# Optimization experiments

Measured on AMD Instinct MI355X. Metric: run time of the kernel, lower is better.

## Reference

```python
import jax, jax.numpy as jnp
import numpy as np

NC, NS, NX, NZ = 128, 2048, 256, 512
B, K = 4, 1
NNZ = NX * NZ * NC  # 16_777_216 nonzeros (~Nc contributions per pixel)


def setup_inputs() -> dict:
    key = jax.random.key(0)
    k1, k2, k3, k4 = jax.random.split(key, 4)
    x = jax.random.normal(k1, (B, K, NC, NS), dtype=jnp.float32)
    csr_vals = jax.random.normal(k2, (NNZ,), dtype=jnp.float32)
    csr_rows = jnp.sort(jax.random.randint(k3, (NNZ,), 0, NX * NZ, dtype=jnp.int64))
    csr_cols = jax.random.randint(k4, (NNZ,), 0, NS * NC, dtype=jnp.int64)
    return {"x": x, "csr_vals": csr_vals, "csr_rows": csr_rows, "csr_cols": csr_cols}


def reference(x, csr_vals, csr_rows, csr_cols):
    # (B,K,Nc,Ns) -> (B,K,Ns,Nc) -> (B*K, Ns*Nc) -> transpose -> (Ns*Nc, B*K)
    rhs = jnp.transpose(x, (0, 1, 3, 2)).reshape(B * K, NS * NC).T
    # SpMM in COO form: out[r, :] += vals * rhs[cols, :]
    gathered = csr_vals[:, None] * rhs[csr_cols]          # (nnz, B*K)
    img_vec = jax.ops.segment_sum(gathered, csr_rows, num_segments=NX * NZ)  # (Nx*Nz, B*K)
    # transpose -> (B*K, Nx*Nz) -> (B,K,Nx,Nz) -> (B,K,Nz,Nx)
    return jnp.transpose(img_vec.T.reshape(B, K, NX, NZ), (0, 1, 3, 2))
```

## Files before the change

kernel.cpp:

```cpp
#include <hip/hip_runtime.h>
#include <hip/hip_fp16.h>

#define NC 128
#define NS 2048
#define NX 256
#define NZ 512
#define NROWS (NX * NZ)
#define NCOLS (NS * NC)
#define RUN 8
#define WAVE_NNZ (RUN * 64)
#define NSLOTS 64


struct alignas(8) Half4 { __half2 lo, hi; };

typedef int   vint4   __attribute__((ext_vector_type(4)));
typedef float vfloat4 __attribute__((ext_vector_type(4)));

__device__ __forceinline__ int4 nt_load_i4(const int* p) {
    vint4 t = __builtin_nontemporal_load((const vint4*)p);
    return make_int4(t.x, t.y, t.z, t.w);
}
__device__ __forceinline__ float4 nt_load_f4(const float* p) {
    vfloat4 t = __builtin_nontemporal_load((const vfloat4*)p);
    return make_float4(t.x, t.y, t.z, t.w);
}

__global__ void pack_rhs_kernel(const float* __restrict__ x,
                                Half4* __restrict__ rhs) {
    int j = blockIdx.x * blockDim.x + threadIdx.x;
    if (j >= NCOLS) return;
    int c = j >> 11;
    int s = j & (NS - 1);
    int base = c * NS + s;
    Half4 h;
    h.lo = __float22half2_rn(make_float2(x[base],               x[base + 1 * NC * NS]));
    h.hi = __float22half2_rn(make_float2(x[base + 2 * NC * NS], x[base + 3 * NC * NS]));
    rhs[s * NC + c] = h;
}

__device__ __forceinline__ void global_flush(float* __restrict__ out, int r, float4 a) {
    int ix = r >> 9;
    int iz = r & (NZ - 1);
    int o = iz * NX + ix;
    atomicAdd(&out[0 * NROWS + o], a.x);
    atomicAdd(&out[1 * NROWS + o], a.y);
    atomicAdd(&out[2 * NROWS + o], a.z);
    atomicAdd(&out[3 * NROWS + o], a.w);
}

__global__ void __launch_bounds__(256, 8) spmm_seg_kernel(
        const float* __restrict__ vals,
        const int* __restrict__ cols,
        const int* __restrict__ rows,
        const Half4* __restrict__ rhs,
        float* __restrict__ out,
        int nnz) {
    __shared__ float sl[4][NSLOTS][4];

    int wv   = threadIdx.x >> 6;
    int lane = threadIdx.x & 63;
    int wid  = (blockIdx.x << 2) + wv;
    int base = wid * WAVE_NNZ + lane * RUN;

    ((float4*)sl)[threadIdx.x] = make_float4(0.f, 0.f, 0.f, 0.f);
    __syncthreads();

    float4 v[2];
    int4   c4[2], r4[2];
    if (base + RUN <= nnz) {
        #pragma unroll
        for (int q = 0; q < 2; ++q) c4[q] = nt_load_i4(cols + base + 4 * q);
        #pragma unroll
        for (int q = 0; q < 2; ++q) v[q]  = nt_load_f4(vals + base + 4 * q);
        #pragma unroll
        for (int q = 0; q < 2; ++q) r4[q] = nt_load_i4(rows + base + 4 * q);
    } else {
        #pragma unroll
        for (int q = 0; q < 2; ++q) {
            #pragma unroll
            for (int k = 0; k < 4; ++k) {
                int e = base + 4 * q + k;
                int ec = e < nnz ? e : (nnz - 1);
                (&v[q].x)[k]  = e < nnz ? vals[ec] : 0.f;
                (&c4[q].x)[k] = cols[ec];
                (&r4[q].x)[k] = rows[ec];
            }
        }
    }

    Half4 g[RUN];
    #pragma unroll
    for (int q = 0; q < 2; ++q) {
        g[4 * q + 0] = rhs[c4[q].x];
        g[4 * q + 1] = rhs[c4[q].y];
        g[4 * q + 2] = rhs[c4[q].z];
        g[4 * q + 3] = rhs[c4[q].w];
    }
    __builtin_amdgcn_sched_barrier(0);

    int rfirst = __shfl(r4[0].x, 0);
    int rlast  = __shfl(r4[1].w, 63);

    int cur = r4[0].x;
    float4 acc = make_float4(0.f, 0.f, 0.f, 0.f);
    #pragma unroll
    for (int j = 0; j < RUN; ++j) {
        int   rj = (&r4[j >> 2].x)[j & 3];
        float vj = (&v[j >> 2].x)[j & 3];
        float2 lo = __half22float2(g[j].lo);
        float2 hi = __half22float2(g[j].hi);
        if (rj != cur) {
            int s = cur - rfirst;
            if (s < NSLOTS) {
                atomicAdd(&sl[wv][s][0], acc.x);
                atomicAdd(&sl[wv][s][1], acc.y);
                atomicAdd(&sl[wv][s][2], acc.z);
                atomicAdd(&sl[wv][s][3], acc.w);
            } else {
                global_flush(out, cur, acc);
            }
            acc = make_float4(0.f, 0.f, 0.f, 0.f);
            cur = rj;
        }
        acc.x += vj * lo.x;
        acc.y += vj * lo.y;
        acc.z += vj * hi.x;
        acc.w += vj * hi.y;
    }
    {
        int s = cur - rfirst;
        if (s < NSLOTS) {
            atomicAdd(&sl[wv][s][0], acc.x);
            atomicAdd(&sl[wv][s][1], acc.y);
            atomicAdd(&sl[wv][s][2], acc.z);
            atomicAdd(&sl[wv][s][3], acc.w);
        } else {
            global_flush(out, cur, acc);
        }
    }

    __syncthreads();

    int span = rlast - rfirst;
    if (lane <= span && lane < NSLOTS) {
        float ax = sl[wv][lane][0];
        float ay = sl[wv][lane][1];
        float az = sl[wv][lane][2];
        float aw = sl[wv][lane][3];
        int rr = rfirst + lane;
        int ix = rr >> 9;
        int iz = rr & (NZ - 1);
        int o = iz * NX + ix;
        if (lane == 0 || rr == rlast) {
            atomicAdd(&out[0 * NROWS + o], ax);
            atomicAdd(&out[1 * NROWS + o], ay);
            atomicAdd(&out[2 * NROWS + o], az);
            atomicAdd(&out[3 * NROWS + o], aw);
        } else {
            out[0 * NROWS + o] = ax;
            out[1 * NROWS + o] = ay;
            out[2 * NROWS + o] = az;
            out[3 * NROWS + o] = aw;
        }
    }
}

__global__ void __launch_bounds__(256) spmm_direct_kernel(
        const float* __restrict__ x,
        const float* __restrict__ vals,
        const int* __restrict__ rows,
        const int* __restrict__ cols,
        int nnz,
        float* __restrict__ out) {
    int r = (blockIdx.x << 2) + (threadIdx.x >> 6);
    int lane = threadIdx.x & 63;
    int start, end;
    {
        int lo = 0, hi = nnz;
        while (lo < hi) { int mid = (lo + hi) >> 1; if (rows[mid] < r) lo = mid + 1; else hi = mid; }
        start = lo;
        hi = nnz;
        int key = r + 1;
        while (lo < hi) { int mid = (lo + hi) >> 1; if (rows[mid] < key) lo = mid + 1; else hi = mid; }
        end = lo;
    }
    float4 acc = {0.f, 0.f, 0.f, 0.f};
    for (int i = start + lane; i < end; i += 64) {
        float v = vals[i];
        int col = cols[i];
        int cc = col & (NC - 1);
        int ss = col >> 7;
        int b = cc * NS + ss;
        acc.x += v * x[b];
        acc.y += v * x[b + 1 * NC * NS];
        acc.z += v * x[b + 2 * NC * NS];
        acc.w += v * x[b + 3 * NC * NS];
    }
    #pragma unroll
    for (int off = 32; off >= 1; off >>= 1) {
        acc.x += __shfl_xor(acc.x, off, 64);
        acc.y += __shfl_xor(acc.y, off, 64);
        acc.z += __shfl_xor(acc.z, off, 64);
        acc.w += __shfl_xor(acc.w, off, 64);
    }
    if (lane < 4) {
        float o = (lane == 0) ? acc.x : (lane == 1) ? acc.y : (lane == 2) ? acc.z : acc.w;
        int ix = r >> 9;
        int iz = r & (NZ - 1);
        out[lane * NROWS + iz * NX + ix] = o;
    }
}

extern "C" void kernel_launch(void* const* d_in, const int* in_sizes, int n_in,
                              void* d_out, int out_size, void* d_ws, size_t ws_size,
                              hipStream_t stream) {
    const float* x        = (const float*)d_in[0];
    const float* csr_vals = (const float*)d_in[1];
    const int*   csr_rows = (const int*)d_in[2];
    const int*   csr_cols = (const int*)d_in[3];
    float* out = (float*)d_out;
    int nnz = in_sizes[1];

    size_t need = (size_t)NCOLS * sizeof(Half4);
    if (ws_size >= need) {
        Half4* rhs = (Half4*)d_ws;
        hipMemsetAsync(out, 0, (size_t)out_size * sizeof(float), stream);
        pack_rhs_kernel<<<(NCOLS + 255) / 256, 256, 0, stream>>>(x, rhs);
        int nblocks = (nnz + 4 * WAVE_NNZ - 1) / (4 * WAVE_NNZ);
        spmm_seg_kernel<<<nblocks, 256, 0, stream>>>(csr_vals, csr_cols, csr_rows,
                                                     rhs, out, nnz);
    } else {
        spmm_direct_kernel<<<NROWS / 4, 256, 0, stream>>>(x, csr_vals, csr_rows, csr_cols, nnz, out);
    }
}
```

Before: 287.6 us.

## Software-pipeline four nnz tiles per wave with double-buffered loads and gathers

Each wave now processes four consecutive 512-nonzero tiles instead of one. The index and value stream loads and the rhs gathers for the next tile are issued before accumulating the current one, using two register buffers. The block-wide barrier is dropped because each wave uses only its own shared-memory slot region. Fewer waves and the occupancy hint lowered from 8 to 4 trade parallelism for per-wave memory-level overlap, at the cost of more register pressure.

```diff
diff --git a/kernel.cpp b/kernel.cpp
--- a/kernel.cpp
+++ b/kernel.cpp
@@ -9,6 +9,8 @@
 #define NCOLS (NS * NC)
 #define RUN 8
 #define WAVE_NNZ (RUN * 64)
+#define NT 4
+#define WAVE_RANGE (NT * WAVE_NNZ)
 #define NSLOTS 64
 
 
@@ -49,38 +51,25 @@
     atomicAdd(&out[3 * NROWS + o], a.w);
 }
 
-__global__ void __launch_bounds__(256, 8) spmm_seg_kernel(
-        const float* __restrict__ vals,
-        const int* __restrict__ cols,
-        const int* __restrict__ rows,
-        const Half4* __restrict__ rhs,
-        float* __restrict__ out,
-        int nnz) {
-    __shared__ float sl[4][NSLOTS][4];
-
-    int wv   = threadIdx.x >> 6;
-    int lane = threadIdx.x & 63;
-    int wid  = (blockIdx.x << 2) + wv;
-    int base = wid * WAVE_NNZ + lane * RUN;
-
-    ((float4*)sl)[threadIdx.x] = make_float4(0.f, 0.f, 0.f, 0.f);
-    __syncthreads();
-
-    float4 v[2];
-    int4   c4[2], r4[2];
-    if (base + RUN <= nnz) {
-        #pragma unroll
-        for (int q = 0; q < 2; ++q) c4[q] = nt_load_i4(cols + base + 4 * q);
-        #pragma unroll
-        for (int q = 0; q < 2; ++q) v[q]  = nt_load_f4(vals + base + 4 * q);
-        #pragma unroll
-        for (int q = 0; q < 2; ++q) r4[q] = nt_load_i4(rows + base + 4 * q);
+__device__ __forceinline__ void load_streams(const float* __restrict__ vals,
+                                             const int* __restrict__ cols,
+                                             const int* __restrict__ rows,
+                                             int nnz, int tb, int lane,
+                                             float4 (&v)[2], int4 (&c4)[2], int4 (&r4)[2]) {
+    int lb = tb + lane * RUN;
+    if (tb + WAVE_NNZ <= nnz) {
+        #pragma unroll
+        for (int q = 0; q < 2; ++q) c4[q] = nt_load_i4(cols + lb + 4 * q);
+        #pragma unroll
+        for (int q = 0; q < 2; ++q) v[q]  = nt_load_f4(vals + lb + 4 * q);
+        #pragma unroll
+        for (int q = 0; q < 2; ++q) r4[q] = nt_load_i4(rows + lb + 4 * q);
     } else {
         #pragma unroll
         for (int q = 0; q < 2; ++q) {
             #pragma unroll
             for (int k = 0; k < 4; ++k) {
-                int e = base + 4 * q + k;
+                int e = lb + 4 * q + k;
                 int ec = e < nnz ? e : (nnz - 1);
                 (&v[q].x)[k]  = e < nnz ? vals[ec] : 0.f;
                 (&c4[q].x)[k] = cols[ec];
@@ -88,8 +77,10 @@
             }
         }
     }
-
-    Half4 g[RUN];
+}
+
+__device__ __forceinline__ void issue_gathers(const Half4* __restrict__ rhs,
+                                              const int4 (&c4)[2], Half4 (&g)[RUN]) {
     #pragma unroll
     for (int q = 0; q < 2; ++q) {
         g[4 * q + 0] = rhs[c4[q].x];
@@ -97,13 +88,13 @@
         g[4 * q + 2] = rhs[c4[q].z];
         g[4 * q + 3] = rhs[c4[q].w];
     }
-    __builtin_amdgcn_sched_barrier(0);
-
-    int rfirst = __shfl(r4[0].x, 0);
-    int rlast  = __shfl(r4[1].w, 63);
-
-    int cur = r4[0].x;
-    float4 acc = make_float4(0.f, 0.f, 0.f, 0.f);
+}
+
+__device__ __forceinline__ void accum_tile(const float4 (&v)[2], const int4 (&r4)[2],
+                                           const Half4 (&g)[RUN],
+                                           int rfirst, int& cur, float4& acc,
+                                           float* __restrict__ out,
+                                           float (*slw)[4]) {
     #pragma unroll
     for (int j = 0; j < RUN; ++j) {
         int   rj = (&r4[j >> 2].x)[j & 3];
@@ -113,10 +104,10 @@
         if (rj != cur) {
             int s = cur - rfirst;
             if (s < NSLOTS) {
-                atomicAdd(&sl[wv][s][0], acc.x);
-                atomicAdd(&sl[wv][s][1], acc.y);
-                atomicAdd(&sl[wv][s][2], acc.z);
-                atomicAdd(&sl[wv][s][3], acc.w);
+                atomicAdd(&slw[s][0], acc.x);
+                atomicAdd(&slw[s][1], acc.y);
+                atomicAdd(&slw[s][2], acc.z);
+                atomicAdd(&slw[s][3], acc.w);
             } else {
                 global_flush(out, cur, acc);
             }
@@ -128,26 +119,82 @@
         acc.z += vj * hi.x;
         acc.w += vj * hi.y;
     }
+}
+
+__global__ void __launch_bounds__(256, 4) spmm_seg_kernel(
+        const float* __restrict__ vals,
+        const int* __restrict__ cols,
+        const int* __restrict__ rows,
+        const Half4* __restrict__ rhs,
+        float* __restrict__ out,
+        int nnz) {
+    __shared__ float sl[4][NSLOTS][4];
+
+    int wv   = threadIdx.x >> 6;
+    int lane = threadIdx.x & 63;
+    int wid  = (blockIdx.x << 2) + wv;
+    int wstart = wid * WAVE_RANGE;
+    if (wstart >= nnz) return;
+    int wend = wstart + WAVE_RANGE;
+    if (wend > nnz) wend = nnz;
+
+    float (*slw)[4] = sl[wv];
+
+    int rfirst = rows[wstart];
+    int rlast  = rows[wend - 1];
+
+    *(float4*)(&slw[lane][0]) = make_float4(0.f, 0.f, 0.f, 0.f);
+
+    float4 v0[2], v1[2];
+    int4   c0[2], c1[2], r0[2], r1[2];
+    Half4  g0[RUN], g1[RUN];
+
+    load_streams(vals, cols, rows, nnz, wstart + 0 * WAVE_NNZ, lane, v0, c0, r0);
+    __builtin_amdgcn_sched_barrier(0);
+    issue_gathers(rhs, c0, g0);
+    __builtin_amdgcn_sched_barrier(0);
+    load_streams(vals, cols, rows, nnz, wstart + 1 * WAVE_NNZ, lane, v1, c1, r1);
+    __builtin_amdgcn_sched_barrier(0);
+
+    int cur = rfirst;
+    float4 acc = make_float4(0.f, 0.f, 0.f, 0.f);
+
+    issue_gathers(rhs, c1, g1);
+    __builtin_amdgcn_sched_barrier(0);
+    accum_tile(v0, r0, g0, rfirst, cur, acc, out, slw);
+    load_streams(vals, cols, rows, nnz, wstart + 2 * WAVE_NNZ, lane, v0, c0, r0);
+    __builtin_amdgcn_sched_barrier(0);
+
+    issue_gathers(rhs, c0, g0);
+    __builtin_amdgcn_sched_barrier(0);
+    accum_tile(v1, r1, g1, rfirst, cur, acc, out, slw);
+    load_streams(vals, cols, rows, nnz, wstart + 3 * WAVE_NNZ, lane, v1, c1, r1);
+    __builtin_amdgcn_sched_barrier(0);
+
+    issue_gathers(rhs, c1, g1);
+    __builtin_amdgcn_sched_barrier(0);
+    accum_tile(v0, r0, g0, rfirst, cur, acc, out, slw);
+
+    accum_tile(v1, r1, g1, rfirst, cur, acc, out, slw);
+
     {
         int s = cur - rfirst;
         if (s < NSLOTS) {
-            atomicAdd(&sl[wv][s][0], acc.x);
-            atomicAdd(&sl[wv][s][1], acc.y);
-            atomicAdd(&sl[wv][s][2], acc.z);
-            atomicAdd(&sl[wv][s][3], acc.w);
+            atomicAdd(&slw[s][0], acc.x);
+            atomicAdd(&slw[s][1], acc.y);
+            atomicAdd(&slw[s][2], acc.z);
+            atomicAdd(&slw[s][3], acc.w);
         } else {
             global_flush(out, cur, acc);
         }
     }
 
-    __syncthreads();
-
     int span = rlast - rfirst;
     if (lane <= span && lane < NSLOTS) {
-        float ax = sl[wv][lane][0];
-        float ay = sl[wv][lane][1];
-        float az = sl[wv][lane][2];
-        float aw = sl[wv][lane][3];
+        float ax = slw[lane][0];
+        float ay = slw[lane][1];
+        float az = slw[lane][2];
+        float aw = slw[lane][3];
         int rr = rfirst + lane;
         int ix = rr >> 9;
         int iz = rr & (NZ - 1);
@@ -227,7 +274,8 @@
         Half4* rhs = (Half4*)d_ws;
         hipMemsetAsync(out, 0, (size_t)out_size * sizeof(float), stream);
         pack_rhs_kernel<<<(NCOLS + 255) / 256, 256, 0, stream>>>(x, rhs);
-        int nblocks = (nnz + 4 * WAVE_NNZ - 1) / (4 * WAVE_NNZ);
+        int per_block = 4 * WAVE_RANGE;
+        int nblocks = (nnz + per_block - 1) / per_block;
         spmm_seg_kernel<<<nblocks, 256, 0, stream>>>(csr_vals, csr_cols, csr_rows,
                                                      rhs, out, nnz);
     } else {
```

Result: no change. 291.8 us (+1.5%).
